# Performance work log

Measured on AMD Instinct MI355X. Metric: run time of the kernel, lower is better.

The kernel has to match this reference:

```python
import jax, jax.numpy as jnp
import numpy as np

B, T = 128, 1024
H1, H2 = 768, 768


def setup_inputs() -> dict:
    key = jax.random.key(0)
    ks = jax.random.split(key, 12)
    s1 = 1.0 / np.sqrt(H1)
    s2 = 1.0 / np.sqrt(H2)
    return {
        "x": jax.random.normal(ks[0], (B, 2, T), dtype=jnp.float32),
        "W_ih1": jax.random.uniform(ks[1], (H1, 2), jnp.float32, -s1, s1),
        "W_hh1": jax.random.uniform(ks[2], (H1, H1), jnp.float32, -s1, s1),
        "b_ih1": jax.random.uniform(ks[3], (H1,), jnp.float32, -s1, s1),
        "b_hh1": jax.random.uniform(ks[4], (H1,), jnp.float32, -s1, s1),
        "W_ih2": jax.random.uniform(ks[5], (H2, H1), jnp.float32, -s2, s2),
        "W_hh2": jax.random.uniform(ks[6], (H2, H2), jnp.float32, -s2, s2),
        "b_ih2": jax.random.uniform(ks[7], (H2,), jnp.float32, -s2, s2),
        "b_hh2": jax.random.uniform(ks[8], (H2,), jnp.float32, -s2, s2),
        "W_lin": jax.random.uniform(ks[9], (2, H2), jnp.float32, -s2, s2),
        "b_lin": jax.random.uniform(ks[10], (2,), jnp.float32, -s2, s2),
        "future": 0,
    }


def reference(x, W_ih1, W_hh1, b_ih1, b_hh1, W_ih2, W_hh2, b_ih2, b_hh2,
              W_lin, b_lin, future):
    Bb = x.shape[0]
    xs = jnp.transpose(x, (2, 0, 1))  # [T, B, 2]

    def cell(xt, ht, W_ih, W_hh, b_ih, b_hh):
        return jnp.tanh(xt @ W_ih.T + b_ih + ht @ W_hh.T + b_hh)

    def step(carry, xt):
        h1, h2 = carry
        h1 = cell(xt, h1, W_ih1, W_hh1, b_ih1, b_hh1)
        h2 = cell(h1, h2, W_ih2, W_hh2, b_ih2, b_hh2)
        out = h2 @ W_lin.T + b_lin  # [B, 2]
        return (h1, h2), out

    h1 = jnp.zeros((Bb, W_hh1.shape[0]), dtype=x.dtype)
    h2 = jnp.zeros((Bb, W_hh2.shape[0]), dtype=x.dtype)
    (h1, h2), outs = jax.lax.scan(step, (h1, h2), xs)  # outs: [T, B, 2]

    if future > 0:
        def fstep(carry, _):
            h1, h2, out = carry
            h1 = cell(out, h1, W_ih1, W_hh1, b_ih1, b_hh1)
            h2 = cell(h1, h2, W_ih2, W_hh2, b_ih2, b_hh2)
            out = h2 @ W_lin.T + b_lin
            return (h1, h2, out), out
        _, fouts = jax.lax.scan(fstep, (h1, h2, outs[-1]), None, length=future)
        outs = jnp.concatenate([outs, fouts], axis=0)

    return jnp.transpose(outs, (1, 2, 0))  # [B, 2, T+future]
```

## Files before the change

kernel.cpp:

```cpp
#include <hip/hip_runtime.h>
#include <math.h>


typedef short s16x8 __attribute__((ext_vector_type(8)));
typedef float fx4   __attribute__((ext_vector_type(4)));

#define NWG    256
#define T_LEN  1024
#define H      768
#define GROUPS 8
#define GROWS  16

#define MAP_OFF    0
#define KBR_OFF    1024
#define GRP_BASE   8192
#define G_FL1  0
#define G_FH2D 128
#define G_FP   256
#define G_EL1  512
#define G_EH2D 2560
#define G_PB   4608
#define G_H1   29184
#define G_H2   422400
#define GRP_STRIDE 520704
#define HB_SZ 24576
#define WS_TOTAL (GRP_BASE + GROUPS * GRP_STRIDE)

__device__ __forceinline__ unsigned short f2bf(float x) {
    unsigned u = __float_as_uint(x);
    unsigned r = (u + 0x7FFFu + ((u >> 16) & 1u)) >> 16;
    return (unsigned short)r;
}
__device__ __forceinline__ float bf2f(unsigned short b) {
    return __uint_as_float(((unsigned)b) << 16);
}
__device__ __forceinline__ fx4 mfma16(s16x8 a, s16x8 b, fx4 c) {
    return __builtin_amdgcn_mfma_f32_16x16x32_bf16(a, b, c, 0, 0, 0);
}

__device__ __forceinline__ void st_ag(unsigned* p, unsigned v) {
    __hip_atomic_store(p, v, __ATOMIC_RELAXED, __HIP_MEMORY_SCOPE_AGENT);
}
__device__ __forceinline__ unsigned ld_ag(const unsigned* p) {
    return __hip_atomic_load(p, __ATOMIC_RELAXED, __HIP_MEMORY_SCOPE_AGENT);
}
__device__ __forceinline__ void acq_ag() {
    __builtin_amdgcn_fence(__ATOMIC_ACQUIRE, "agent");
}
__device__ __forceinline__ void st32_sc0(unsigned* p, unsigned v) {
    asm volatile("global_store_dword %0, %1, off sc0" :: "v"(p), "v"(v) : "memory");
}
__device__ __forceinline__ void stflag_l2(unsigned* p, unsigned v) {
    asm volatile("global_atomic_swap %0, %1, off" :: "v"(p), "v"(v) : "memory");
}
__device__ __forceinline__ void umax_l2(unsigned* p, unsigned v) {
    asm volatile("global_atomic_umax %0, %1, off" :: "v"(p), "v"(v) : "memory");
}
__device__ __forceinline__ unsigned rdflag_l2(unsigned* p) {
    unsigned v, z = 0;
    asm volatile("global_atomic_add %0, %1, %2, off sc0\n\ts_waitcnt vmcnt(0)"
                 : "=v"(v) : "v"(p), "v"(z) : "memory");
    return v;
}
__device__ __forceinline__ void inv_l1() {
    asm volatile("buffer_inv sc0" ::: "memory");
}

template<bool LOCAL> __device__ __forceinline__ unsigned rdp(unsigned* p) {
    if constexpr (LOCAL) return rdflag_l2(p); else return ld_ag(p);
}
template<bool LOCAL> __device__ __forceinline__ void std32(unsigned* p, unsigned v) {
    if constexpr (LOCAL) st32_sc0(p, v); else st_ag(p, v);
}

__device__ __forceinline__ void load_wfrag(const float* __restrict__ W,
                                           int col, int kk, s16x8& hi, s16x8& lo) {
    const float* p = W + (long)col * H + kk;
#pragma unroll
    for (int j = 0; j < 8; j++) {
        float w = p[j];
        unsigned short h = f2bf(w);
        float r = w - bf2f(h);
        hi[j] = (short)h;
        lo[j] = (short)f2bf(r);
    }
}

__device__ __forceinline__ void ld6(const unsigned short* p, s16x8 (&d)[6]) {
#pragma unroll
    for (int ks = 0; ks < 6; ks++)
        d[ks] = *reinterpret_cast<const s16x8*>(p + ks * 32);
}

__device__ __forceinline__ unsigned wave_min(unsigned v) {
#pragma unroll
    for (int o = 32; o; o >>= 1) {
        unsigned u = (unsigned)__shfl_xor((int)v, o);
        v = v < u ? v : u;
    }
    return v;
}

__device__ __forceinline__ void arrive_pub(unsigned* own, unsigned ownval,
                                           unsigned* raw, int n, int ownidx,
                                           unsigned* reps, int tid) {
    if (tid == 0) stflag_l2(own, ownval);
    if (tid < 64) {
        asm volatile("s_waitcnt vmcnt(0)" ::: "memory");
        unsigned v = 0xFFFFFFFFu;
        if (tid < n) v = (tid == ownidx) ? ownval : rdflag_l2(raw + tid);
        unsigned m = wave_min(v);
        if (m >= ownval && tid < 32) umax_l2(reps + tid * 16, m);
    }
}

__device__ __forceinline__ unsigned wait_ep(unsigned* reps, unsigned* raw, int n,
                                            unsigned T, int tid, int lrank,
                                            unsigned cached, bool do_inv,
                                            volatile unsigned* sh) {
    if (cached < T) {
        if (tid < 64) {
            unsigned* myrep = reps + lrank * 16;
            unsigned m = 0;
            long spin = 0;
            for (;;) {
                if ((spin & 7) == 7) {
                    unsigned v = (tid < n) ? rdflag_l2(raw + tid) : 0xFFFFFFFFu;
                    m = wave_min(v);
                } else {
                    if (tid == 0) m = rdflag_l2(myrep);
                    m = (unsigned)__shfl((int)m, 0);
                }
                if (m >= T) break;
                __builtin_amdgcn_s_sleep(1);
                if (++spin > (1L << 20)) break;
            }
            if (tid == 0) *sh = m;
        }
    }
    if (do_inv && tid == 0) inv_l1();
    __syncthreads();
    return (cached < T) ? *sh : cached;
}

__device__ __forceinline__ unsigned wait_raw(unsigned* raw, int n, unsigned T,
                                             int tid, unsigned cached,
                                             volatile unsigned* sh) {
    if (cached < T) {
        if (tid < 64) {
            unsigned m;
            long spin = 0;
            for (;;) {
                unsigned v = (tid < n) ? rdflag_l2(raw + tid) : 0xFFFFFFFFu;
                m = wave_min(v);
                if (m >= T) break;
                __builtin_amdgcn_s_sleep(1);
                if (++spin > (1L << 20)) break;
            }
            if (tid == 0) *sh = m;
        }
    }
    __syncthreads();
    return (cached < T) ? *sh : cached;
}

__device__ __forceinline__ void wait_agent(unsigned* f, int n, unsigned T,
                                           int tid, bool acquire) {
    if (tid < 64) {
        int l = tid < n ? tid : n - 1;
        long spin = 0;
        for (;;) {
            if (wave_min(ld_ag(f + l)) >= T) break;
            __builtin_amdgcn_s_sleep(1);
            if (++spin > (1L << 20)) break;
        }
    }
    if (acquire && tid == 0) acq_ag();
    __syncthreads();
}

#define DRAIN() do { asm volatile("s_waitcnt vmcnt(0)" ::: "memory"); __syncthreads(); } while (0)

template<bool LOCAL>
__device__ __forceinline__ void run_group(
    int group, int lrank, int tid, int lane, int w, int l15, int lk8,
    const float* __restrict__ x,
    const float* __restrict__ Wih1, const float* __restrict__ Whh1,
    const float* __restrict__ bih1, const float* __restrict__ bhh1,
    const float* __restrict__ Wih2, const float* __restrict__ Whh2,
    const float* __restrict__ bih2, const float* __restrict__ bhh2,
    const float* __restrict__ Wlin, const float* __restrict__ blin,
    float* __restrict__ out, unsigned char* __restrict__ gb,
    float (*red)[16][97], volatile unsigned* shm)
{
    unsigned* fL1  = (unsigned*)(gb + G_FL1);
    unsigned* fH2d = (unsigned*)(gb + G_FH2D);
    unsigned* fP   = (unsigned*)(gb + G_FP);
    unsigned* eL1  = (unsigned*)(gb + G_EL1);
    unsigned* eH2d = (unsigned*)(gb + G_EH2D);
    float*    Pb   = (float*)(gb + G_PB);
    const int kb0 = w * 192;

    if (lrank < 8) {
        const int c = lrank;
        const int col0 = c * 96;

        s16x8 whi[6][6], wlo[6][6];
#pragma unroll
        for (int ks = 0; ks < 6; ks++)
#pragma unroll
            for (int nt = 0; nt < 6; nt++)
                load_wfrag(Whh1, col0 + nt * 16 + l15, kb0 + ks * 32 + lk8,
                           whi[ks][nt], wlo[ks][nt]);

        const int er = tid >> 4;
        const int ec0 = (tid & 15) * 6;
        const int b = group * GROWS + er;
        float bs[6], wi0[6], wi1[6];
#pragma unroll
        for (int j = 0; j < 6; j++) {
            int cg = col0 + ec0 + j;
            bs[j] = bih1[cg] + bhh1[cg];
            wi0[j] = Wih1[cg * 2 + 0];
            wi1[j] = Wih1[cg * 2 + 1];
        }
        const int ov = tid >> 5;
        const int oj = tid & 31;
        const int orow = 2 * c + (ov >> 1);
        const int ooo = ov & 1;
        const float blv = blin[ooo];

        unsigned fpc = 0, fl1c = 0;

        for (int t = 0; t < T_LEN; t++) {
            const int rs = (t + 7) & 7;
            const int wsl = t & 7;
            float x0 = x[b * 2048 + t];
            float x1 = x[b * 2048 + 1024 + t];

            if (t >= 7) {
                if constexpr (LOCAL)
                    fpc = wait_raw(fP, 24, (unsigned)(t - 6), tid, fpc, &shm[0]);
                else
                    wait_agent(fP, 24, (unsigned)(t - 6), tid, false);
                if (tid < 128) {
                    float p = 0.f;
                    if (oj < 24)
                        p = __uint_as_float(rdp<LOCAL>((unsigned*)
                            (Pb + ((((t - 7) & 7) * 16 + orow) * 2 + ooo) * 24 + oj)));
#pragma unroll
                    for (int o = 16; o; o >>= 1) p += __shfl_down(p, o, 32);
                    if (oj == 0) out[(group * GROWS + orow) * 2048 + ooo * 1024 + (t - 7)] = p + blv;
                }
            }

            if (t) {
                if constexpr (LOCAL)
                    fl1c = wait_ep(eL1, fL1, 8, (unsigned)t, tid, lrank, fl1c, true, &shm[1]);
                else
                    wait_agent(fL1, 8, (unsigned)t, tid, true);
            }

            const unsigned short* Hh = (const unsigned short*)(gb + G_H1 + rs * 2 * HB_SZ);
            const unsigned short* Hl = (const unsigned short*)(gb + G_H1 + rs * 2 * HB_SZ + HB_SZ);
            s16x8 ah[6], al[6];
            ld6(Hh + l15 * H + kb0 + lk8, ah);
            ld6(Hl + l15 * H + kb0 + lk8, al);

            fx4 acc[6];
#pragma unroll
            for (int nt = 0; nt < 6; nt++) acc[nt] = fx4{0.f, 0.f, 0.f, 0.f};
#pragma unroll
            for (int ks = 0; ks < 6; ks++)
#pragma unroll
                for (int nt = 0; nt < 6; nt++) {
                    acc[nt] = mfma16(ah[ks], whi[ks][nt], acc[nt]);
                    acc[nt] = mfma16(ah[ks], wlo[ks][nt], acc[nt]);
                    acc[nt] = mfma16(al[ks], whi[ks][nt], acc[nt]);
                }

#pragma unroll
            for (int nt = 0; nt < 6; nt++)
#pragma unroll
                for (int i = 0; i < 4; i++)
                    red[w][(lane >> 4) * 4 + i][nt * 16 + l15] = acc[nt][i];
            __syncthreads();

            unsigned hw[3], lw[3];
#pragma unroll
            for (int jj = 0; jj < 3; jj++) {
                unsigned hp = 0, lp = 0;
#pragma unroll
                for (int k = 0; k < 2; k++) {
                    int j = jj * 2 + k;
                    int cc = ec0 + j;
                    float v = red[0][er][cc] + red[1][er][cc] + red[2][er][cc] + red[3][er][cc];
                    v += x0 * wi0[j] + x1 * wi1[j] + bs[j];
                    v = tanhf(v);
                    unsigned short hb = f2bf(v);
                    unsigned short lb = f2bf(v - bf2f(hb));
                    hp |= ((unsigned)hb) << (16 * k);
                    lp |= ((unsigned)lb) << (16 * k);
                }
                hw[jj] = hp; lw[jj] = lp;
            }

            unsigned* Dh = (unsigned*)(gb + G_H1 + wsl * 2 * HB_SZ) + ((long)er * H + col0 + ec0) / 2;
            unsigned* Dl = (unsigned*)(gb + G_H1 + wsl * 2 * HB_SZ + HB_SZ) + ((long)er * H + col0 + ec0) / 2;
            std32<LOCAL>(Dh + 0, hw[0]); std32<LOCAL>(Dh + 1, hw[1]); std32<LOCAL>(Dh + 2, hw[2]);
            std32<LOCAL>(Dl + 0, lw[0]); std32<LOCAL>(Dl + 1, lw[1]); std32<LOCAL>(Dl + 2, lw[2]);

            DRAIN();
            if constexpr (LOCAL)
                arrive_pub(fL1 + c, (unsigned)(t + 1), fL1, 8, c, eL1, tid);
            else if (tid == 0)
                st_ag(fL1 + c, (unsigned)(t + 1));
        }

        if constexpr (LOCAL)
            fpc = wait_raw(fP, 24, (unsigned)T_LEN, tid, fpc, &shm[0]);
        else
            wait_agent(fP, 24, (unsigned)T_LEN, tid, false);
        if (tid < 128) {
#pragma unroll
            for (int par = 0; par < 7; par++) {
                int tt = T_LEN - 7 + par;
                float p = 0.f;
                if (oj < 24)
                    p = __uint_as_float(rdp<LOCAL>((unsigned*)
                        (Pb + (((tt & 7) * 16 + orow) * 2 + ooo) * 24 + oj)));
#pragma unroll
                for (int o = 16; o; o >>= 1) p += __shfl_down(p, o, 32);
                if (oj == 0) out[(group * GROWS + orow) * 2048 + ooo * 1024 + tt] = p + blv;
            }
        }
    } else {
        const int q = lrank - 8;
        const int col0 = q * 32;

        s16x8 ghi[2][6], glo[2][6], ihi[2][6], ilo[2][6];
#pragma unroll
        for (int nt = 0; nt < 2; nt++)
#pragma unroll
            for (int ks = 0; ks < 6; ks++) {
                load_wfrag(Whh2, col0 + nt * 16 + l15, kb0 + ks * 32 + lk8, ghi[nt][ks], glo[nt][ks]);
                load_wfrag(Wih2, col0 + nt * 16 + l15, kb0 + ks * 32 + lk8, ihi[nt][ks], ilo[nt][ks]);
            }

        const int er = tid >> 4;
        const int ec0 = (tid & 15) * 2;
        const float bsA = bih2[col0 + ec0] + bhh2[col0 + ec0];
        const float bsB = bih2[col0 + ec0 + 1] + bhh2[col0 + ec0 + 1];

        const int ro = tid >> 1, oo = tid & 1;
        float wl[32];
        if (tid < 32) {
#pragma unroll
            for (int cc = 0; cc < 32; cc++) wl[cc] = Wlin[oo * H + col0 + cc];
        }

        unsigned fh2c = 0, fl1c = 0;

        for (int t = 0; t < T_LEN; t++) {
            const int rb = (t + 1) & 1;
            const int wb = t & 1;
            const int hs = t & 7;

            if (t) {
                if constexpr (LOCAL)
                    fh2c = wait_ep(eH2d, fH2d, 24, (unsigned)t, tid, lrank, fh2c, true, &shm[2]);
                else
                    wait_agent(fH2d, 24, (unsigned)t, tid, true);
            }

            const unsigned short* Gh = (const unsigned short*)(gb + G_H2 + rb * 2 * HB_SZ);
            const unsigned short* Gl = (const unsigned short*)(gb + G_H2 + rb * 2 * HB_SZ + HB_SZ);
            const unsigned short* Hh = (const unsigned short*)(gb + G_H1 + hs * 2 * HB_SZ);
            const unsigned short* Hl = (const unsigned short*)(gb + G_H1 + hs * 2 * HB_SZ + HB_SZ);

            s16x8 ah[6], al[6], bh[6], bl[6];
            bool h1rdy = false;
            if constexpr (LOCAL) h1rdy = (fl1c >= (unsigned)(t + 1));

            ld6(Gh + l15 * H + kb0 + lk8, ah);
            ld6(Gl + l15 * H + kb0 + lk8, al);
            if (h1rdy) {
                ld6(Hh + l15 * H + kb0 + lk8, bh);
                ld6(Hl + l15 * H + kb0 + lk8, bl);
            }

            fx4 a2[2];
            a2[0] = fx4{0.f, 0.f, 0.f, 0.f};
            a2[1] = fx4{0.f, 0.f, 0.f, 0.f};
#pragma unroll
            for (int ks = 0; ks < 6; ks++)
#pragma unroll
                for (int nt = 0; nt < 2; nt++) {
                    a2[nt] = mfma16(ah[ks], ghi[nt][ks], a2[nt]);
                    a2[nt] = mfma16(ah[ks], glo[nt][ks], a2[nt]);
                    a2[nt] = mfma16(al[ks], ghi[nt][ks], a2[nt]);
                }

            if (!h1rdy) {
                if constexpr (LOCAL)
                    fl1c = wait_ep(eL1, fL1, 8, (unsigned)(t + 1), tid, lrank, fl1c, false, &shm[3]);
                else
                    wait_agent(fL1, 8, (unsigned)(t + 1), tid, true);
                ld6(Hh + l15 * H + kb0 + lk8, bh);
                ld6(Hl + l15 * H + kb0 + lk8, bl);
            }

#pragma unroll
            for (int ks = 0; ks < 6; ks++)
#pragma unroll
                for (int nt = 0; nt < 2; nt++) {
                    a2[nt] = mfma16(bh[ks], ihi[nt][ks], a2[nt]);
                    a2[nt] = mfma16(bh[ks], ilo[nt][ks], a2[nt]);
                    a2[nt] = mfma16(bl[ks], ihi[nt][ks], a2[nt]);
                }

#pragma unroll
            for (int nt = 0; nt < 2; nt++)
#pragma unroll
                for (int i = 0; i < 4; i++)
                    red[w][(lane >> 4) * 4 + i][nt * 16 + l15] = a2[nt][i];
            __syncthreads();

            float v0 = red[0][er][ec0] + red[1][er][ec0] + red[2][er][ec0] + red[3][er][ec0] + bsA;
            float v1 = red[0][er][ec0 + 1] + red[1][er][ec0 + 1] + red[2][er][ec0 + 1] + red[3][er][ec0 + 1] + bsB;
            v0 = tanhf(v0); v1 = tanhf(v1);
            unsigned short hb0 = f2bf(v0), hb1 = f2bf(v1);
            unsigned hp = ((unsigned)hb0) | (((unsigned)hb1) << 16);
            unsigned lp = ((unsigned)f2bf(v0 - bf2f(hb0))) | (((unsigned)f2bf(v1 - bf2f(hb1))) << 16);
            unsigned* Dh = (unsigned*)(gb + G_H2 + wb * 2 * HB_SZ) + ((long)er * H + col0 + ec0) / 2;
            unsigned* Dl = (unsigned*)(gb + G_H2 + wb * 2 * HB_SZ + HB_SZ) + ((long)er * H + col0 + ec0) / 2;
            std32<LOCAL>(Dh, hp);
            std32<LOCAL>(Dl, lp);
            red[0][er][ec0] = v0;
            red[0][er][ec0 + 1] = v1;

            DRAIN();
            if constexpr (LOCAL)
                arrive_pub(fH2d + q, (unsigned)(t + 1), fH2d, 24, q, eH2d, tid);
            else if (tid == 0)
                st_ag(fH2d + q, (unsigned)(t + 1));

            if (tid < 32) {
                float s = 0.f;
#pragma unroll
                for (int cc = 0; cc < 32; cc++) s += red[0][ro][cc] * wl[cc];
                std32<LOCAL>((unsigned*)&Pb[(((t & 7) * 16 + ro) * 2 + oo) * 24 + q],
                             __float_as_uint(s));
            }

            DRAIN();
            if (tid == 0) {
                if constexpr (LOCAL) stflag_l2(fP + q, (unsigned)(t + 1));
                else st_ag(fP + q, (unsigned)(t + 1));
            }
        }
    }
}

__global__ __launch_bounds__(256, 1) void rnn_persist(
    const float* __restrict__ x,
    const float* __restrict__ Wih1, const float* __restrict__ Whh1,
    const float* __restrict__ bih1, const float* __restrict__ bhh1,
    const float* __restrict__ Wih2, const float* __restrict__ Whh2,
    const float* __restrict__ bih2, const float* __restrict__ bhh2,
    const float* __restrict__ Wlin, const float* __restrict__ blin,
    float* __restrict__ out, unsigned char* __restrict__ ws)
{
    const int wg = blockIdx.x;
    const int tid = threadIdx.x;
    const int lane = tid & 63;
    const int w = tid >> 6;
    const int l15 = lane & 15;
    const int lk8 = (lane >> 4) * 8;

    __shared__ float red[4][16][97];
    __shared__ int iscr[256];
    __shared__ unsigned shm[4];

    unsigned* map = (unsigned*)(ws + MAP_OFF);
    unsigned* kbr = (unsigned*)(ws + KBR_OFF);

    int key;
    asm volatile("s_getreg_b32 %0, hwreg(HW_REG_XCC_ID, 0, 4)" : "=s"(key));
    key &= 0xF;

    if (tid == 0) st_ag(map + wg, (unsigned)(key + 1));
    unsigned kj;
    {
        long spin = 0;
        for (;;) {
            kj = ld_ag(map + tid);
            if (kj) break;
            __builtin_amdgcn_s_sleep(2);
            if (++spin > (1L << 20)) break;
        }
    }
    int contrib = (((int)kj - 1) < key || (((int)kj - 1) == key && tid < wg)) ? 1 : 0;
    iscr[tid] = contrib;
    __syncthreads();
#pragma unroll
    for (int s = 128; s; s >>= 1) {
        if (tid < s) iscr[tid] += iscr[tid + s];
        __syncthreads();
    }
    const int rank = iscr[0];
    __syncthreads();
    const int group = rank >> 5, lrank = rank & 31;

    if (tid == 0) st_ag(kbr + rank, (unsigned)(key + 1));
    unsigned kv;
    {
        long spin = 0;
        for (;;) {
            kv = ld_ag(kbr + tid);
            if (kv) break;
            __builtin_amdgcn_s_sleep(2);
            if (++spin > (1L << 20)) break;
        }
    }
    int eq = ((int)kv - 1 == key) ? 1 : 0;
    int bad = ((tid >> 5) == group && !eq) ? 1 : 0;
    iscr[tid] = eq | (bad << 16);
    __syncthreads();
#pragma unroll
    for (int s = 128; s; s >>= 1) {
        if (tid < s) iscr[tid] += iscr[tid + s];
        __syncthreads();
    }
    const int r0 = iscr[0];
    __syncthreads();
    const bool local = ((r0 & 0xFFFF) == 32) && ((r0 >> 16) == 0);

    unsigned char* gb = ws + GRP_BASE + (size_t)group * GRP_STRIDE;

    if (local)
        run_group<true>(group, lrank, tid, lane, w, l15, lk8,
                        x, Wih1, Whh1, bih1, bhh1, Wih2, Whh2, bih2, bhh2,
                        Wlin, blin, out, gb, red, shm);
    else
        run_group<false>(group, lrank, tid, lane, w, l15, lk8,
                         x, Wih1, Whh1, bih1, bhh1, Wih2, Whh2, bih2, bhh2,
                         Wlin, blin, out, gb, red, shm);
}

extern "C" void kernel_launch(void* const* d_in, const int* in_sizes, int n_in,
                              void* d_out, int out_size, void* d_ws, size_t ws_size,
                              hipStream_t stream) {
    const float* x    = (const float*)d_in[0];
    const float* Wih1 = (const float*)d_in[1];
    const float* Whh1 = (const float*)d_in[2];
    const float* bih1 = (const float*)d_in[3];
    const float* bhh1 = (const float*)d_in[4];
    const float* Wih2 = (const float*)d_in[5];
    const float* Whh2 = (const float*)d_in[6];
    const float* bih2 = (const float*)d_in[7];
    const float* bhh2 = (const float*)d_in[8];
    const float* Wlin = (const float*)d_in[9];
    const float* blin = (const float*)d_in[10];

    hipMemsetAsync(d_ws, 0, WS_TOTAL, stream);

    rnn_persist<<<NWG, 256, 0, stream>>>(x, Wih1, Whh1, bih1, bhh1,
                                         Wih2, Whh2, bih2, bhh2,
                                         Wlin, blin, (float*)d_out,
                                         (unsigned char*)d_ws);
}
```

Baseline: 6.130 ms.

## Replace representative-flag barrier with per-wave waits on padded producer flags

```diff
diff --git a/kernel.cpp b/kernel.cpp
--- a/kernel.cpp
+++ b/kernel.cpp
@@ -15,13 +15,11 @@
 #define KBR_OFF    1024
 #define GRP_BASE   8192
 #define G_FL1  0
-#define G_FH2D 128
-#define G_FP   256
-#define G_EL1  512
-#define G_EH2D 2560
-#define G_PB   4608
-#define G_H1   29184
-#define G_H2   422400
+#define G_FH2D 512
+#define G_FP   2048
+#define G_PB   3584
+#define G_H1   28160
+#define G_H2   421376
 #define GRP_STRIDE 520704
 #define HB_SZ 24576
 #define WS_TOTAL (GRP_BASE + GROUPS * GRP_STRIDE)
@@ -52,9 +50,6 @@
 }
 __device__ __forceinline__ void stflag_l2(unsigned* p, unsigned v) {
     asm volatile("global_atomic_swap %0, %1, off" :: "v"(p), "v"(v) : "memory");
-}
-__device__ __forceinline__ void umax_l2(unsigned* p, unsigned v) {
-    asm volatile("global_atomic_umax %0, %1, off" :: "v"(p), "v"(v) : "memory");
 }
 __device__ __forceinline__ unsigned rdflag_l2(unsigned* p) {
     unsigned v, z = 0;
@@ -101,67 +96,39 @@
     return v;
 }
 
-__device__ __forceinline__ void arrive_pub(unsigned* own, unsigned ownval,
-                                           unsigned* raw, int n, int ownidx,
-                                           unsigned* reps, int tid) {
-    if (tid == 0) stflag_l2(own, ownval);
-    if (tid < 64) {
-        asm volatile("s_waitcnt vmcnt(0)" ::: "memory");
-        unsigned v = 0xFFFFFFFFu;
-        if (tid < n) v = (tid == ownidx) ? ownval : rdflag_l2(raw + tid);
-        unsigned m = wave_min(v);
-        if (m >= ownval && tid < 32) umax_l2(reps + tid * 16, m);
-    }
-}
-
-__device__ __forceinline__ unsigned wait_ep(unsigned* reps, unsigned* raw, int n,
-                                            unsigned T, int tid, int lrank,
-                                            unsigned cached, bool do_inv,
-                                            volatile unsigned* sh) {
-    if (cached < T) {
-        if (tid < 64) {
-            unsigned* myrep = reps + lrank * 16;
-            unsigned m = 0;
-            long spin = 0;
-            for (;;) {
-                if ((spin & 7) == 7) {
-                    unsigned v = (tid < n) ? rdflag_l2(raw + tid) : 0xFFFFFFFFu;
-                    m = wave_min(v);
-                } else {
-                    if (tid == 0) m = rdflag_l2(myrep);
-                    m = (unsigned)__shfl((int)m, 0);
-                }
-                if (m >= T) break;
-                __builtin_amdgcn_s_sleep(1);
-                if (++spin > (1L << 20)) break;
-            }
-            if (tid == 0) *sh = m;
-        }
-    }
-    if (do_inv && tid == 0) inv_l1();
-    __syncthreads();
-    return (cached < T) ? *sh : cached;
-}
-
-__device__ __forceinline__ unsigned wait_raw(unsigned* raw, int n, unsigned T,
+__device__ __forceinline__ unsigned wait_wv(unsigned* f, int n, unsigned T,
+                                            int lane, unsigned cached) {
+    if (cached >= T) return cached;
+    unsigned m;
+    long spin = 0;
+    for (;;) {
+        unsigned v = (lane < n) ? rdflag_l2(f + lane * 16) : 0xFFFFFFFFu;
+        m = wave_min(v);
+        if (m >= T) break;
+        __builtin_amdgcn_s_sleep(1);
+        if (++spin > (1L << 20)) break;
+    }
+    return m;
+}
+
+__device__ __forceinline__ unsigned gate_raw(unsigned* raw, int n, unsigned T,
                                              int tid, unsigned cached,
                                              volatile unsigned* sh) {
-    if (cached < T) {
-        if (tid < 64) {
-            unsigned m;
-            long spin = 0;
-            for (;;) {
-                unsigned v = (tid < n) ? rdflag_l2(raw + tid) : 0xFFFFFFFFu;
-                m = wave_min(v);
-                if (m >= T) break;
-                __builtin_amdgcn_s_sleep(1);
-                if (++spin > (1L << 20)) break;
-            }
-            if (tid == 0) *sh = m;
-        }
+    if (cached >= T) return cached;
+    if (tid < 64) {
+        unsigned m;
+        long spin = 0;
+        for (;;) {
+            unsigned v = (tid < n) ? rdflag_l2(raw + tid * 16) : 0xFFFFFFFFu;
+            m = wave_min(v);
+            if (m >= T) break;
+            __builtin_amdgcn_s_sleep(1);
+            if (++spin > (1L << 20)) break;
+        }
+        if (tid == 0) *sh = m;
     }
     __syncthreads();
-    return (cached < T) ? *sh : cached;
+    return *sh;
 }
 
 __device__ __forceinline__ void wait_agent(unsigned* f, int n, unsigned T,
@@ -170,7 +137,7 @@
         int l = tid < n ? tid : n - 1;
         long spin = 0;
         for (;;) {
-            if (wave_min(ld_ag(f + l)) >= T) break;
+            if (wave_min(ld_ag(f + l * 16)) >= T) break;
             __builtin_amdgcn_s_sleep(1);
             if (++spin > (1L << 20)) break;
         }
@@ -196,8 +163,6 @@
     unsigned* fL1  = (unsigned*)(gb + G_FL1);
     unsigned* fH2d = (unsigned*)(gb + G_FH2D);
     unsigned* fP   = (unsigned*)(gb + G_FP);
-    unsigned* eL1  = (unsigned*)(gb + G_EL1);
-    unsigned* eH2d = (unsigned*)(gb + G_EH2D);
     float*    Pb   = (float*)(gb + G_PB);
     const int kb0 = w * 192;
 
@@ -230,7 +195,8 @@
         const int ooo = ov & 1;
         const float blv = blin[ooo];
 
-        unsigned fpc = 0, fl1c = 0;
+        unsigned fpc = 0;
+        unsigned fl1w = 0;
 
         for (int t = 0; t < T_LEN; t++) {
             const int rs = (t + 7) & 7;
@@ -240,7 +206,7 @@
 
             if (t >= 7) {
                 if constexpr (LOCAL)
-                    fpc = wait_raw(fP, 24, (unsigned)(t - 6), tid, fpc, &shm[0]);
+                    fpc = gate_raw(fP, 24, (unsigned)(t - 6), tid, fpc, &shm[0]);
                 else
                     wait_agent(fP, 24, (unsigned)(t - 6), tid, false);
                 if (tid < 128) {
@@ -255,10 +221,12 @@
             }
 
             if (t) {
-                if constexpr (LOCAL)
-                    fl1c = wait_ep(eL1, fL1, 8, (unsigned)t, tid, lrank, fl1c, true, &shm[1]);
-                else
+                if constexpr (LOCAL) {
+                    fl1w = wait_wv(fL1 + 2 * w * 16, 2, (unsigned)t, lane, fl1w);
+                    inv_l1();
+                } else {
                     wait_agent(fL1, 8, (unsigned)t, tid, true);
+                }
             }
 
             const unsigned short* Hh = (const unsigned short*)(gb + G_H1 + rs * 2 * HB_SZ);
@@ -311,14 +279,14 @@
             std32<LOCAL>(Dl + 0, lw[0]); std32<LOCAL>(Dl + 1, lw[1]); std32<LOCAL>(Dl + 2, lw[2]);
 
             DRAIN();
-            if constexpr (LOCAL)
-                arrive_pub(fL1 + c, (unsigned)(t + 1), fL1, 8, c, eL1, tid);
-            else if (tid == 0)
-                st_ag(fL1 + c, (unsigned)(t + 1));
+            if (tid == 0) {
+                if constexpr (LOCAL) stflag_l2(fL1 + c * 16, (unsigned)(t + 1));
+                else st_ag(fL1 + c * 16, (unsigned)(t + 1));
+            }
         }
 
         if constexpr (LOCAL)
-            fpc = wait_raw(fP, 24, (unsigned)T_LEN, tid, fpc, &shm[0]);
+            fpc = gate_raw(fP, 24, (unsigned)T_LEN, tid, fpc, &shm[0]);
         else
             wait_agent(fP, 24, (unsigned)T_LEN, tid, false);
         if (tid < 128) {
@@ -359,7 +327,7 @@
             for (int cc = 0; cc < 32; cc++) wl[cc] = Wlin[oo * H + col0 + cc];
         }
 
-        unsigned fh2c = 0, fl1c = 0;
+        unsigned fh2w = 0, fl1w = 0;
 
         for (int t = 0; t < T_LEN; t++) {
             const int rb = (t + 1) & 1;
@@ -368,9 +336,14 @@
 
             if (t) {
                 if constexpr (LOCAL)
-                    fh2c = wait_ep(eH2d, fH2d, 24, (unsigned)t, tid, lrank, fh2c, true, &shm[2]);
+                    fh2w = wait_wv(fH2d + 6 * w * 16, 6, (unsigned)t, lane, fh2w);
                 else
                     wait_agent(fH2d, 24, (unsigned)t, tid, true);
+            }
+            bool h1rdy = false;
+            if constexpr (LOCAL) {
+                inv_l1();
+                h1rdy = (fl1w >= (unsigned)(t + 1));
             }
 
             const unsigned short* Gh = (const unsigned short*)(gb + G_H2 + rb * 2 * HB_SZ);
@@ -379,9 +352,6 @@
             const unsigned short* Hl = (const unsigned short*)(gb + G_H1 + hs * 2 * HB_SZ + HB_SZ);
 
             s16x8 ah[6], al[6], bh[6], bl[6];
-            bool h1rdy = false;
-            if constexpr (LOCAL) h1rdy = (fl1c >= (unsigned)(t + 1));
-
             ld6(Gh + l15 * H + kb0 + lk8, ah);
             ld6(Gl + l15 * H + kb0 + lk8, al);
             if (h1rdy) {
@@ -402,10 +372,11 @@
                 }
 
             if (!h1rdy) {
-                if constexpr (LOCAL)
-                    fl1c = wait_ep(eL1, fL1, 8, (unsigned)(t + 1), tid, lrank, fl1c, false, &shm[3]);
-                else
+                if constexpr (LOCAL) {
+                    fl1w = wait_wv(fL1 + 2 * w * 16, 2, (unsigned)(t + 1), lane, fl1w);
+                } else {
                     wait_agent(fL1, 8, (unsigned)(t + 1), tid, true);
+                }
                 ld6(Hh + l15 * H + kb0 + lk8, bh);
                 ld6(Hl + l15 * H + kb0 + lk8, bl);
             }
@@ -440,10 +411,10 @@
             red[0][er][ec0 + 1] = v1;
 
             DRAIN();
-            if constexpr (LOCAL)
-                arrive_pub(fH2d + q, (unsigned)(t + 1), fH2d, 24, q, eH2d, tid);
-            else if (tid == 0)
-                st_ag(fH2d + q, (unsigned)(t + 1));
+            if (tid == 0) {
+                if constexpr (LOCAL) stflag_l2(fH2d + q * 16, (unsigned)(t + 1));
+                else st_ag(fH2d + q * 16, (unsigned)(t + 1));
+            }
 
             if (tid < 32) {
                 float s = 0.f;
@@ -455,8 +426,8 @@
 
             DRAIN();
             if (tid == 0) {
-                if constexpr (LOCAL) stflag_l2(fP + q, (unsigned)(t + 1));
-                else st_ag(fP + q, (unsigned)(t + 1));
+                if constexpr (LOCAL) stflag_l2(fP + q * 16, (unsigned)(t + 1));
+                else st_ag(fP + q * 16, (unsigned)(t + 1));
             }
         }
     }
```

New measurement: 5.223 ms. 14.8% less time.
